# Performance work log

Measured on AMD Instinct MI355X. Metric: run time of the kernel, lower is better.

## Reference

```python
import jax, jax.numpy as jnp
import numpy as np
from functools import partial

V, H, B, T, L = 32000, 1024, 64, 64, 4
EOS = 2


def setup_inputs() -> dict:
    key = jax.random.key(0)
    ks = jax.random.split(key, 10)
    s = 1.0 / np.sqrt(H)
    return {
        "max_len": T,
        "tgt": jax.random.randint(ks[0], (B, T), 0, V),
        "h0": jax.random.normal(ks[1], (L, B, H), jnp.float32),
        "c0": jax.random.normal(ks[2], (L, B, H), jnp.float32),
        "embedding": jax.random.normal(ks[3], (V, H), jnp.float32) * s,
        "W_ih": jax.random.normal(ks[4], (L, 4 * H, H), jnp.float32) * s,
        "W_hh": jax.random.normal(ks[5], (L, 4 * H, H), jnp.float32) * s,
        "b_ih": jax.random.normal(ks[6], (L, 4 * H), jnp.float32) * s,
        "b_hh": jax.random.normal(ks[7], (L, 4 * H), jnp.float32) * s,
        "W_cls": jax.random.normal(ks[8], (V, H), jnp.float32) * s,
        "b_cls": jax.random.normal(ks[9], (V,), jnp.float32) * s,
    }


def _lstm_cell(x, h, c, Wi, Wh, bi, bh):
    # gates: [B, 4H] in torch order (i, f, g, o)
    g = x @ Wi.T + bi + h @ Wh.T + bh
    i, f, gg, o = jnp.split(g, 4, axis=-1)
    c2 = jax.nn.sigmoid(f) * c + jax.nn.sigmoid(i) * jnp.tanh(gg)
    h2 = jax.nn.sigmoid(o) * jnp.tanh(c2)
    return h2, c2


def reference(max_len, tgt, h0, c0, embedding, W_ih, W_hh, b_ih, b_hh, W_cls, b_cls):
    # step i>0 uses embedding of tgt[:, i-1].
    batch = tgt.shape[0]
    x0 = jnp.broadcast_to(embedding[EOS], (batch, embedding.shape[1]))
    tf_in = embedding[tgt[:, : max_len - 1]]              # [B, T-1, H]
    inputs = jnp.concatenate([x0[:, None, :], tf_in], axis=1)  # [B, T, H]
    inputs = jnp.swapaxes(inputs, 0, 1)                   # [T, B, H]

    def step(carry, x):
        h, c = carry  # each [L, B, H]
        hs, cs = [], []
        inp = x
        for l in range(L):  # 4 stacked LSTM cells, h of cell l feeds cell l+1
            hn, cn = _lstm_cell(inp, h[l], c[l], W_ih[l], W_hh[l], b_ih[l], b_hh[l])
            hs.append(hn)
            cs.append(cn)
            inp = hn
        h = jnp.stack(hs)
        c = jnp.stack(cs)
        logp = jax.nn.log_softmax(h[L - 1] @ W_cls.T + b_cls, axis=-1)  # [B, V]
        return (h, c), logp

    (h, c), out = jax.lax.scan(step, (h0, c0), inputs)
    return out, h, c  # out: [T, B, V]
```

## Files before the change

### kernel.cpp

```cpp
#include <hip/hip_runtime.h>

using u16 = unsigned short;
using u32 = unsigned int;

typedef __bf16 bf16x8 __attribute__((ext_vector_type(8)));
typedef float  f32x4  __attribute__((ext_vector_type(4)));
typedef u16    u16x8  __attribute__((ext_vector_type(8)));

static constexpr int kV = 32000, kH = 1024, kB = 64, kT = 64, kL = 4, kEOS = 2;

struct Flag { int v; int pad[15]; };

__device__ __forceinline__ u16 f2bf(float f) {
  u32 u = __float_as_uint(f);
  u = (u + 0x7fffu + ((u >> 16) & 1u)) >> 16;
  return (u16)u;
}
__device__ __forceinline__ float sigf(float x)   { return 1.0f / (1.0f + __expf(-x)); }
__device__ __forceinline__ float tanhf_(float x) { return 1.0f - 2.0f / (__expf(2.0f * x) + 1.0f); }

typedef const __attribute__((address_space(1))) u32* gas_ptr;
typedef __attribute__((address_space(3))) u32*       las_ptr;
__device__ __forceinline__ void async16(const u16* g, u16* l) {
  __builtin_amdgcn_global_load_lds((gas_ptr)g, (las_ptr)l, 16, 0, 0);
}

__device__ __forceinline__ void spin_ge(const int* p, int tgt) {
  while (__hip_atomic_load(p, __ATOMIC_RELAXED, __HIP_MEMORY_SCOPE_AGENT) < tgt)
    __builtin_amdgcn_s_sleep(2);
}

__device__ __forceinline__ size_t packed_off(int b, int k) {
  return (size_t)(((b >> 4) * 32 + (k >> 5)) * 512 + (((k >> 3) & 3) * 16 + (b & 15)) * 8 + (k & 7));
}


__global__ void pack_lstm(const float* __restrict__ Wih, const float* __restrict__ Whh,
                          u16* __restrict__ wpack) {
  const int cid  = blockIdx.x * 256 + threadIdx.x;
  const int lane = cid & 63;
  const int cf   = (cid >> 6) & 3;
  const int kk   = (cid >> 8) & 31;
  const int mt   = (cid >> 13) & 1;
  const int blk  = cid >> 14;
  const int lay = blk >> 6, cb = blk & 63;
  const int wr = cf * 1024 + cb * 16 + (lane & 15);
  const int kb = kk * 32 + (lane >> 4) * 8;
  const float* src = (mt ? Whh : Wih) + ((size_t)lay * 4096 + wr) * 1024 + kb;
  const float4* s4 = (const float4*)src;
  float4 v0 = s4[0], v1 = s4[1];
  u16x8 r;
  r[0]=f2bf(v0.x); r[1]=f2bf(v0.y); r[2]=f2bf(v0.z); r[3]=f2bf(v0.w);
  r[4]=f2bf(v1.x); r[5]=f2bf(v1.y); r[6]=f2bf(v1.z); r[7]=f2bf(v1.w);
  *(u16x8*)(wpack + (size_t)cid * 8) = r;
}

__global__ void pack_cls(const float* __restrict__ W, u16* __restrict__ o) {
  const int cid = blockIdx.x * 256 + threadIdx.x;
  const int bn  = cid >> 14;
  const int rem = cid & 16383;
  const int kk  = rem >> 9;
  const int p   = rem & 511;
  const int l4  = p >> 7;
  const int row = p & 127;
  const float* src = W + ((size_t)(bn * 128 + row)) * 1024 + kk * 32 + l4 * 8;
  const float4* s4 = (const float4*)src;
  float4 v0 = s4[0], v1 = s4[1];
  u16x8 r;
  r[0]=f2bf(v0.x); r[1]=f2bf(v0.y); r[2]=f2bf(v0.z); r[3]=f2bf(v0.w);
  r[4]=f2bf(v1.x); r[5]=f2bf(v1.y); r[6]=f2bf(v1.z); r[7]=f2bf(v1.w);
  *(u16x8*)(o + (size_t)cid * 8) = r;
}

__global__ void pack_x(const float* __restrict__ emb, const int* __restrict__ tgt,
                       u16* __restrict__ X) {
  const int cid = blockIdx.x * 256 + threadIdx.x;
  const int kc = cid & 127, b = (cid >> 7) & 63, t = cid >> 13;
  const int tok = (t == 0) ? kEOS : tgt[b * 64 + t - 1];
  const float4* s4 = (const float4*)(emb + (size_t)tok * 1024 + kc * 8);
  float4 v0 = s4[0], v1 = s4[1];
  u16x8 r;
  r[0]=f2bf(v0.x); r[1]=f2bf(v0.y); r[2]=f2bf(v0.z); r[3]=f2bf(v0.w);
  r[4]=f2bf(v1.x); r[5]=f2bf(v1.y); r[6]=f2bf(v1.z); r[7]=f2bf(v1.w);
  *(u16x8*)(X + (size_t)t * 65536 + packed_off(b, kc * 8)) = r;
}

__global__ void pack_init(const float* __restrict__ h0, const float* __restrict__ bih,
                          const float* __restrict__ bhh, u16* __restrict__ hball,
                          float* __restrict__ bsum) {
  const int cid = blockIdx.x * 256 + threadIdx.x;
  if (cid < 32768) {
    const int kc = cid & 127, row = cid >> 7;
    const int lay = row >> 6, b = row & 63;
    const float4* s4 = (const float4*)(h0 + (size_t)cid * 8);
    float4 v0 = s4[0], v1 = s4[1];
    u16x8 r;
    r[0]=f2bf(v0.x); r[1]=f2bf(v0.y); r[2]=f2bf(v0.z); r[3]=f2bf(v0.w);
    r[4]=f2bf(v1.x); r[5]=f2bf(v1.y); r[6]=f2bf(v1.z); r[7]=f2bf(v1.w);
    *(u16x8*)(hball + (size_t)lay * 65 * 65536 + packed_off(b, kc * 8)) = r;
  } else {
    const int i = cid - 32768;
    bsum[i] = bih[i] + bhh[i];
  }
}

__global__ void __launch_bounds__(1024, 4)
lstm_coop(const u16* __restrict__ wpack, const u16* __restrict__ xall,
          u16* __restrict__ hball, const float* __restrict__ bsum,
          const float* __restrict__ c0, float* __restrict__ outh, float* __restrict__ outc,
          Flag* flags) {
  __shared__ u16 stg[3][32][512];
  __shared__ float Gc[2][64][80];

  const int tid = threadIdx.x, lane = tid & 63, wave = tid >> 6;
  const int l15 = lane & 15, l4 = lane >> 4;
  const int cmat = wave >> 3, cwc = (wave >> 1) & 3, ckh = wave & 1;
  const int blk = blockIdx.x;
  const int lay = (blk >> 1) & 3;
  const int cb  = ((blk >> 3) << 1) | (blk & 1);
  const int u0 = cb << 4;
  const int ub = tid >> 4, uu = tid & 15;

  float creg = c0[((size_t)lay * 64 + ub) * 1024 + u0 + uu];
  float bsv[4];
  #pragma unroll
  for (int g = 0; g < 4; ++g) bsv[g] = bsum[lay * 4096 + g * 1024 + u0 + uu];

  const size_t wbase = (size_t)(lay * 64 + cb) * 131072;
  bf16x8 breg[16];
  #pragma unroll
  for (int j = 0; j < 16; ++j)
    breg[j] = *(const bf16x8*)(wpack + wbase
        + (size_t)(((cmat * 32 + 2 * j + ckh) * 4) + cwc) * 512 + lane * 8);

  const int j0 = wave * 2, j1 = wave * 2 + 1;
  const int m2a = j0 >> 4, mta = (j0 >> 2) & 3, ksla = j0 & 3;
  const int m2b = j1 >> 4, mtb = (j1 >> 2) & 3, kslb = j1 & 3;

  u16* hlay = hball + (size_t)lay * 65 * 65536;
  const u16* hprev = (lay == 0) ? xall : (hball + (size_t)(lay - 1) * 65 * 65536);

  #pragma unroll 1
  for (int t = 0; t < kT; ++t) {
    if (t > 0 && tid < 64)                 spin_ge(&flags[lay * 64 + tid].v, t);
    if (lay > 0 && tid >= 64 && tid < 128) spin_ge(&flags[(lay - 1) * 64 + (tid - 64)].v, t + 1);
    __syncthreads();

    const u16* xsrc = (lay == 0) ? (xall + (size_t)t * 65536)
                                 : (hprev + (size_t)(t + 1) * 65536);
    const u16* hsrc = hlay + (size_t)t * 65536;

    const u16* ga = (m2a ? hsrc : xsrc) + (size_t)((mta * 32 + ksla) * 512) + lane * 8;
    const u16* gb = (m2b ? hsrc : xsrc) + (size_t)((mtb * 32 + kslb) * 512) + lane * 8;

    auto STAGE = [&](int c) {
      async16(ga + (size_t)c * 2048, &stg[c % 3][m2a * 16 + mta * 4 + ksla][0]);
      async16(gb + (size_t)c * 2048, &stg[c % 3][m2b * 16 + mtb * 4 + kslb][0]);
    };

    f32x4 acc[4] = {};
    STAGE(0); STAGE(1);
    #pragma unroll
    for (int c = 0; c < 8; ++c) {
      if (c < 7) asm volatile("s_waitcnt vmcnt(2)" ::: "memory");
      else       asm volatile("s_waitcnt vmcnt(0)" ::: "memory");
      __builtin_amdgcn_s_barrier();
      asm volatile("" ::: "memory");
      if (c < 6) STAGE(c + 2);
      const u16* As = &stg[c % 3][cmat * 16][0];
      #pragma unroll
      for (int s = 0; s < 2; ++s) {
        const int ksl = 2 * s + ckh;
        bf16x8 a[4];
        #pragma unroll
        for (int m = 0; m < 4; ++m)
          a[m] = *(const bf16x8*)(As + (m * 4 + ksl) * 512 + lane * 8);
        #pragma unroll
        for (int m = 0; m < 4; ++m)
          acc[m] = __builtin_amdgcn_mfma_f32_16x16x32_bf16(a[m], breg[2 * c + s], acc[m], 0, 0, 0);
      }
    }

    if (ckh == 0) {
      #pragma unroll
      for (int m = 0; m < 4; ++m)
        #pragma unroll
        for (int r = 0; r < 4; ++r)
          Gc[cmat][m * 16 + l4 * 4 + r][cwc * 16 + l15] = acc[m][r];
    }
    __syncthreads();
    if (ckh == 1) {
      #pragma unroll
      for (int m = 0; m < 4; ++m)
        #pragma unroll
        for (int r = 0; r < 4; ++r)
          Gc[cmat][m * 16 + l4 * 4 + r][cwc * 16 + l15] += acc[m][r];
    }
    __syncthreads();

    float sg[4];
    #pragma unroll
    for (int g = 0; g < 4; ++g) {
      const int col = g * 16 + uu;
      sg[g] = Gc[0][ub][col] + Gc[1][ub][col] + bsv[g];
    }
    const float c2 = sigf(sg[1]) * creg + sigf(sg[0]) * tanhf_(sg[2]);
    const float h2 = sigf(sg[3]) * tanhf_(c2);
    creg = c2;
    const u16 hv = f2bf(h2);
    if (t == kT - 1) {
      outh[((size_t)lay * 64 + ub) * 1024 + u0 + uu] = h2;
      outc[((size_t)lay * 64 + ub) * 1024 + u0 + uu] = c2;
    }
    const u32 other = __shfl_xor((u32)hv, 1);
    if ((tid & 1) == 0) {
      const u32 hpair = (u32)hv | (other << 16);
      u32* hdst = (u32*)(hlay + (size_t)(t + 1) * 65536 + packed_off(ub, u0 + uu));
      __hip_atomic_store(hdst, hpair, __ATOMIC_RELAXED, __HIP_MEMORY_SCOPE_AGENT);
    }
    __syncthreads();
    if (tid == 0)
      __hip_atomic_store(&flags[lay * 64 + cb].v, t + 1, __ATOMIC_RELAXED, __HIP_MEMORY_SCOPE_AGENT);
  }
}

#define CLS_EPILOGUE()                                                                     \
  {                                                                                        \
    float* sRm = (float*)&sA[0][0];                                          \
    float* sRs = sRm + 256;                                                                \
    _Pragma("unroll")                                                                      \
    for (int mi = 0; mi < 4; ++mi) {                                                       \
      _Pragma("unroll")                                                                    \
      for (int r = 0; r < 4; ++r) {                                                        \
        float v[4];                                                                        \
        _Pragma("unroll")                                                                  \
        for (int ci = 0; ci < 4; ++ci) v[ci] = acc[mi][ci][r] + bc[ci];                     \
        float mx = fmaxf(fmaxf(v[0], v[1]), fmaxf(v[2], v[3]));                            \
        mx = fmaxf(mx, __shfl_xor(mx, 1)); mx = fmaxf(mx, __shfl_xor(mx, 2));              \
        mx = fmaxf(mx, __shfl_xor(mx, 4)); mx = fmaxf(mx, __shfl_xor(mx, 8));              \
        float ss = __expf(v[0]-mx) + __expf(v[1]-mx) + __expf(v[2]-mx) + __expf(v[3]-mx);  \
        ss += __shfl_xor(ss, 1); ss += __shfl_xor(ss, 2);                                  \
        ss += __shfl_xor(ss, 4); ss += __shfl_xor(ss, 8);                                  \
        const int lr = wm * 64 + mi * 16 + l4 * 4 + r;                                     \
        if (l15 == 0) { sRm[wc * 128 + lr] = mx; sRs[wc * 128 + lr] = ss; }                \
      }                                                                                    \
    }                                                                                      \
    __syncthreads();                                                                       \
    if (tid < 128) {                                                                       \
      const float m0 = sRm[tid], s0 = sRs[tid];                                            \
      const float m1 = sRm[128 + tid], s1 = sRs[128 + tid];                                \
      const float M = fmaxf(m0, m1);                                                       \
      const float S = s0 * __expf(m0 - M) + s1 * __expf(m1 - M);                           \
      pmax[(size_t)(bm * 128 + tid) * 256 + bn] = M;                                       \
      psum[(size_t)(bm * 128 + tid) * 256 + bn] = S;                                       \
    }                                                                                      \
  }

__global__ void __launch_bounds__(256)
cls_gemm(const u16* __restrict__ A, const u16* __restrict__ Bw,
         const float* __restrict__ bcls, float* __restrict__ out,
         float* __restrict__ pmax, float* __restrict__ psum) {
  __shared__ u16 sA[3][4096], sB[3][4096];
  const int tid = threadIdx.x, lane = tid & 63, wave = tid >> 6;
  const int wm = wave >> 1, wc = wave & 1;
  const int l15 = lane & 15, l4 = lane >> 4;
  const int bm = blockIdx.x, bn = blockIdx.y;
  const u16* Ab = A  + (size_t)bm * 131072;
  const u16* Bb = Bw + (size_t)bn * 131072;

  auto STAGE = [&](int kk) {
    u16* dA = sA[kk % 3]; u16* dB = sB[kk % 3];
    #pragma unroll
    for (int q = 0; q < 4; ++q) {
      const int u = wave * 4 + q;
      if (u < 8) {
        const u16* g = Ab + (size_t)(u >> 2) * 65536 + (size_t)(((u & 3) * 32 + kk) * 512) + lane * 8;
        async16(g, dA + u * 512);
      } else {
        const int v = u & 7;
        const u16* g = Bb + (size_t)kk * 4096 + v * 512 + lane * 8;
        async16(g, dB + v * 512);
      }
    }
  };

  f32x4 acc[4][4] = {};
  STAGE(0); STAGE(1);
  for (int kk = 0; kk < 32; ++kk) {
    if (kk < 31) asm volatile("s_waitcnt vmcnt(4)" ::: "memory");
    else         asm volatile("s_waitcnt vmcnt(0)" ::: "memory");
    __builtin_amdgcn_s_barrier();
    asm volatile("" ::: "memory");
    if (kk < 30) STAGE(kk + 2);
    const u16* aS = sA[kk % 3]; const u16* bS = sB[kk % 3];
    bf16x8 av[4], bv[4];
    #pragma unroll
    for (int mi = 0; mi < 4; ++mi) av[mi] = *(const bf16x8*)(aS + (wm * 4 + mi) * 512 + lane * 8);
    #pragma unroll
    for (int ci = 0; ci < 4; ++ci) bv[ci] = *(const bf16x8*)(bS + l4 * 1024 + (wc * 64 + ci * 16 + l15) * 8);
    #pragma unroll
    for (int mi = 0; mi < 4; ++mi)
      #pragma unroll
      for (int ci = 0; ci < 4; ++ci)
        acc[mi][ci] = __builtin_amdgcn_mfma_f32_16x16x32_bf16(av[mi], bv[ci], acc[mi][ci], 0, 0, 0);
  }
  float bc[4];
  #pragma unroll
  for (int ci = 0; ci < 4; ++ci) bc[ci] = bcls[bn * 128 + wc * 64 + ci * 16 + l15];
  #pragma unroll
  for (int ci = 0; ci < 4; ++ci) {
    const int col = bn * 128 + wc * 64 + ci * 16 + l15;
    #pragma unroll
    for (int mi = 0; mi < 4; ++mi)
      #pragma unroll
      for (int r = 0; r < 4; ++r) {
        const int row = bm * 128 + wm * 64 + mi * 16 + l4 * 4 + r;
        out[(size_t)row * 32000 + col] = acc[mi][ci][r] + bc[ci];
      }
  }
  __syncthreads();
  CLS_EPILOGUE()
}

__global__ void __launch_bounds__(256)
cls_gemm_f32(const u16* __restrict__ A, const float* __restrict__ Bw,
             const float* __restrict__ bcls, float* __restrict__ out,
             float* __restrict__ pmax, float* __restrict__ psum) {
  __shared__ u16 sA[3][4096], sB[3][4096];
  const int tid = threadIdx.x, lane = tid & 63, wave = tid >> 6;
  const int wm = wave >> 1, wc = wave & 1;
  const int l15 = lane & 15, l4 = lane >> 4;
  const int bm = blockIdx.x, bn = blockIdx.y;
  const u16*  Ab = A  + (size_t)bm * 131072;
  const float* Bb = Bw + (size_t)bn * 131072;

  auto LOADB = [&](int kk, u16x8* rb) {
    #pragma unroll
    for (int q = 0; q < 2; ++q) {
      const int p = tid + q * 256, row = p & 127, khi = p >> 7;
      const float4* s4 = (const float4*)(Bb + (size_t)row * 1024 + kk * 32 + khi * 8);
      float4 v0 = s4[0], v1 = s4[1];
      u16x8 r;
      r[0]=f2bf(v0.x); r[1]=f2bf(v0.y); r[2]=f2bf(v0.z); r[3]=f2bf(v0.w);
      r[4]=f2bf(v1.x); r[5]=f2bf(v1.y); r[6]=f2bf(v1.z); r[7]=f2bf(v1.w);
      rb[q] = r;
    }
  };
  auto WRITEB = [&](int kk, const u16x8* rb) {
    u16* dB = sB[kk % 3];
    #pragma unroll
    for (int q = 0; q < 2; ++q) {
      const int p = tid + q * 256, row = p & 127, khi = p >> 7;
      *(u16x8*)(dB + khi * 1024 + row * 8) = rb[q];
    }
  };
  auto STAGE_A = [&](int kk) {
    u16* dA = sA[kk % 3];
    #pragma unroll
    for (int q = 0; q < 2; ++q) {
      const int v = wave * 2 + q;
      const u16* g = Ab + (size_t)(v >> 2) * 65536 + (size_t)(((v & 3) * 32 + kk) * 512) + lane * 8;
      async16(g, dA + v * 512);
    }
  };

  f32x4 acc[4][4] = {};
  {
    u16x8 rb[2];
    LOADB(0, rb); STAGE_A(0); WRITEB(0, rb);
  }
  for (int kk = 0; kk < 32; ++kk) {
    if (kk < 31) {
      u16x8 rb[2];
      LOADB(kk + 1, rb);
      STAGE_A(kk + 1);
      WRITEB(kk + 1, rb);
    } else {
      asm volatile("s_waitcnt vmcnt(0)" ::: "memory");
    }
    __builtin_amdgcn_s_barrier();
    asm volatile("" ::: "memory");
    const u16* aS = sA[kk % 3]; const u16* bS = sB[kk % 3];
    bf16x8 av[4], bv[4];
    #pragma unroll
    for (int mi = 0; mi < 4; ++mi) av[mi] = *(const bf16x8*)(aS + (wm * 4 + mi) * 512 + lane * 8);
    #pragma unroll
    for (int ci = 0; ci < 4; ++ci) bv[ci] = *(const bf16x8*)(bS + l4 * 1024 + (wc * 64 + ci * 16 + l15) * 8);
    #pragma unroll
    for (int mi = 0; mi < 4; ++mi)
      #pragma unroll
      for (int ci = 0; ci < 4; ++ci)
        acc[mi][ci] = __builtin_amdgcn_mfma_f32_16x16x32_bf16(av[mi], bv[ci], acc[mi][ci], 0, 0, 0);
    asm volatile("" ::: "memory");
    __builtin_amdgcn_s_barrier();
  }
  float bc[4];
  #pragma unroll
  for (int ci = 0; ci < 4; ++ci) bc[ci] = bcls[bn * 128 + wc * 64 + ci * 16 + l15];
  #pragma unroll
  for (int ci = 0; ci < 4; ++ci) {
    const int col = bn * 128 + wc * 64 + ci * 16 + l15;
    #pragma unroll
    for (int mi = 0; mi < 4; ++mi)
      #pragma unroll
      for (int r = 0; r < 4; ++r) {
        const int row = bm * 128 + wm * 64 + mi * 16 + l4 * 4 + r;
        out[(size_t)row * 32000 + col] = acc[mi][ci][r] + bc[ci];
      }
  }
  __syncthreads();
  CLS_EPILOGUE()
}

__global__ void __launch_bounds__(256)
lsm_red(const float* __restrict__ pmax, const float* __restrict__ psum,
        float* __restrict__ logz) {
  __shared__ float rm[256], rs[256];
  const int r = blockIdx.x, b = threadIdx.x;
  float m = -3.0e38f, s = 0.0f;
  if (b < 250) { m = pmax[(size_t)r * 256 + b]; s = psum[(size_t)r * 256 + b]; }
  rm[b] = m; rs[b] = s; __syncthreads();
  for (int st = 128; st > 0; st >>= 1) {
    if (b < st) {
      const float m2 = rm[b + st], s2 = rs[b + st];
      const float M = fmaxf(rm[b], m2);
      rs[b] = rs[b] * __expf(rm[b] - M) + s2 * __expf(m2 - M);
      rm[b] = M;
    }
    __syncthreads();
  }
  if (b == 0) logz[r] = rm[0] + logf(rs[0]);
}

__global__ void __launch_bounds__(256)
sub_k(float* __restrict__ out, const float* __restrict__ logz) {
  const int r = blockIdx.x;
  const float z = logz[r];
  float4* p = (float4*)(out + (size_t)r * 32000);
  for (int v = threadIdx.x; v < 8000; v += 256) {
    float4 x = p[v];
    x.x -= z; x.y -= z; x.z -= z; x.w -= z;
    p[v] = x;
  }
}

extern "C" void kernel_launch(void* const* d_in, const int* in_sizes, int n_in,
                              void* d_out, int out_size, void* d_ws, size_t ws_size,
                              hipStream_t stream) {
  (void)in_sizes; (void)n_in; (void)out_size;
  const int*   tgt  = (const int*)d_in[1];
  const float* h0   = (const float*)d_in[2];
  const float* c0   = (const float*)d_in[3];
  const float* emb  = (const float*)d_in[4];
  const float* Wih  = (const float*)d_in[5];
  const float* Whh  = (const float*)d_in[6];
  const float* bih  = (const float*)d_in[7];
  const float* bhh  = (const float*)d_in[8];
  const float* Wcls = (const float*)d_in[9];
  const float* bcls = (const float*)d_in[10];

  float* out  = (float*)d_out;
  float* outh = out + (size_t)kT * kB * kV;
  float* outc = outh + (size_t)kL * kB * kH;

  const size_t SZ_WPACK = 67108864;
  const size_t SZ_WCLS  = 65536000;
  const size_t SZ_X     = 8388608;
  const size_t SZ_HBALL = 34078720;
  const size_t SZ_BSUM  = 65536;
  const size_t SZ_FLAGS = 16384;
  const size_t SZ_PM    = 4194304;
  const size_t FULL_REQ = SZ_WPACK + SZ_WCLS + SZ_X + SZ_HBALL + SZ_BSUM + SZ_FLAGS + 2 * SZ_PM + 16384;
  const bool full = (ws_size >= FULL_REQ);

  char* ws = (char*)d_ws;
  size_t off = 0;
  u16* wpack = (u16*)(ws + off); off += SZ_WPACK;
  u16* wclsb = nullptr;
  if (full) { wclsb = (u16*)(ws + off); off += SZ_WCLS; }
  u16*   X     = (u16*)(ws + off); off += SZ_X;
  u16*   hball = (u16*)(ws + off); off += SZ_HBALL;
  float* bsum  = (float*)(ws + off); off += SZ_BSUM;
  Flag*  flags = (Flag*)(ws + off);  off += SZ_FLAGS;
  float* pmax  = (float*)(ws + off); off += SZ_PM;
  float* psum  = (float*)(ws + off); off += SZ_PM;
  float* logz  = (float*)(ws + off); off += 16384;

  pack_lstm<<<16384, 256, 0, stream>>>(Wih, Whh, wpack);
  if (full) pack_cls<<<16000, 256, 0, stream>>>(Wcls, wclsb);
  pack_x   <<<2048,  256, 0, stream>>>(emb, tgt, X);
  pack_init<<<192,   256, 0, stream>>>(h0, bih, bhh, hball, bsum);
  hipMemsetAsync(flags, 0, SZ_FLAGS, stream);

  void* args[] = { (void*)&wpack, (void*)&X, (void*)&hball, (void*)&bsum,
                   (void*)&c0, (void*)&outh, (void*)&outc, (void*)&flags };
  hipLaunchCooperativeKernel((const void*)lstm_coop, dim3(256), dim3(1024), args, 0, stream);

  const u16* h3a = hball + (size_t)3 * 65 * 65536 + 65536;
  if (full) cls_gemm    <<<dim3(32, 250), 256, 0, stream>>>(h3a, wclsb, bcls, out, pmax, psum);
  else      cls_gemm_f32<<<dim3(32, 250), 256, 0, stream>>>(h3a, Wcls,  bcls, out, pmax, psum);
  lsm_red<<<4096, 256, 0, stream>>>(pmax, psum, logz);
  sub_k  <<<4096, 256, 0, stream>>>(out, logz);
}
```

Measured before the change: 1.263 ms.

## Enlarge classifier GEMM M-tile to 256 rows and fuse logsumexp reduce with subtract

The bf16 classifier GEMM now computes 256x128 output tiles per block instead of 128x128. Each wave holds 8x4 MFMA accumulators, which halves how often the W_cls tiles are reloaded and halves the grid along M. The log-softmax row reduction and the logZ subtraction are merged into one kernel, removing one launch and the logz round trip. The cost is more registers and LDS per block, which may lower occupancy.

```diff
diff --git a/kernel.cpp b/kernel.cpp
--- a/kernel.cpp
+++ b/kernel.cpp
@@ -224,9 +224,104 @@
   }
 }
 
-#define CLS_EPILOGUE()                                                                     \
+__global__ void __launch_bounds__(256, 2)
+cls_gemm(const u16* __restrict__ A, const u16* __restrict__ Bw,
+         const float* __restrict__ bcls, float* __restrict__ out,
+         float* __restrict__ pmax, float* __restrict__ psum) {
+  __shared__ u16 sA[3][8192], sB[3][4096];
+  const int tid = threadIdx.x, lane = tid & 63, wave = tid >> 6;
+  const int wm = wave >> 1, wc = wave & 1;
+  const int l15 = lane & 15, l4 = lane >> 4;
+  const int bm = blockIdx.x, bn = blockIdx.y;
+  const u16* Ab = A  + (size_t)bm * 262144;
+  const u16* Bb = Bw + (size_t)bn * 131072;
+
+  auto STAGE = [&](int kk) {
+    u16* dA = sA[kk % 3]; u16* dB = sB[kk % 3];
+    #pragma unroll
+    for (int q = 0; q < 6; ++q) {
+      const int u = wave * 6 + q;
+      if (u < 16) {
+        const u16* g = Ab + (size_t)(u >> 2) * 65536 + (size_t)(((u & 3) * 32 + kk) * 512) + lane * 8;
+        async16(g, dA + u * 512);
+      } else {
+        const int v = u - 16;
+        const u16* g = Bb + (size_t)kk * 4096 + v * 512 + lane * 8;
+        async16(g, dB + v * 512);
+      }
+    }
+  };
+
+  f32x4 acc[8][4] = {};
+  STAGE(0); STAGE(1);
+  for (int kk = 0; kk < 32; ++kk) {
+    if (kk < 31) asm volatile("s_waitcnt vmcnt(6)" ::: "memory");
+    else         asm volatile("s_waitcnt vmcnt(0)" ::: "memory");
+    __builtin_amdgcn_s_barrier();
+    asm volatile("" ::: "memory");
+    if (kk < 30) STAGE(kk + 2);
+    const u16* aS = sA[kk % 3]; const u16* bS = sB[kk % 3];
+    bf16x8 av[8], bv[4];
+    #pragma unroll
+    for (int mi = 0; mi < 8; ++mi) av[mi] = *(const bf16x8*)(aS + (size_t)(wm * 8 + mi) * 512 + lane * 8);
+    #pragma unroll
+    for (int ci = 0; ci < 4; ++ci) bv[ci] = *(const bf16x8*)(bS + l4 * 1024 + (wc * 64 + ci * 16 + l15) * 8);
+    #pragma unroll
+    for (int mi = 0; mi < 8; ++mi)
+      #pragma unroll
+      for (int ci = 0; ci < 4; ++ci)
+        acc[mi][ci] = __builtin_amdgcn_mfma_f32_16x16x32_bf16(av[mi], bv[ci], acc[mi][ci], 0, 0, 0);
+  }
+  float bc[4];
+  #pragma unroll
+  for (int ci = 0; ci < 4; ++ci) bc[ci] = bcls[bn * 128 + wc * 64 + ci * 16 + l15];
+  #pragma unroll
+  for (int ci = 0; ci < 4; ++ci) {
+    const int col = bn * 128 + wc * 64 + ci * 16 + l15;
+    #pragma unroll
+    for (int mi = 0; mi < 8; ++mi)
+      #pragma unroll
+      for (int r = 0; r < 4; ++r) {
+        const int row = bm * 256 + wm * 128 + mi * 16 + l4 * 4 + r;
+        out[(size_t)row * 32000 + col] = acc[mi][ci][r] + bc[ci];
+      }
+  }
+  __syncthreads();
+  {
+    float* sRm = (float*)&sA[0][0];
+    float* sRs = sRm + 512;
+    #pragma unroll
+    for (int mi = 0; mi < 8; ++mi) {
+      #pragma unroll
+      for (int r = 0; r < 4; ++r) {
+        float v[4];
+        #pragma unroll
+        for (int ci = 0; ci < 4; ++ci) v[ci] = acc[mi][ci][r] + bc[ci];
+        float mx = fmaxf(fmaxf(v[0], v[1]), fmaxf(v[2], v[3]));
+        mx = fmaxf(mx, __shfl_xor(mx, 1)); mx = fmaxf(mx, __shfl_xor(mx, 2));
+        mx = fmaxf(mx, __shfl_xor(mx, 4)); mx = fmaxf(mx, __shfl_xor(mx, 8));
+        float ss = __expf(v[0]-mx) + __expf(v[1]-mx) + __expf(v[2]-mx) + __expf(v[3]-mx);
+        ss += __shfl_xor(ss, 1); ss += __shfl_xor(ss, 2);
+        ss += __shfl_xor(ss, 4); ss += __shfl_xor(ss, 8);
+        const int lr = wm * 128 + mi * 16 + l4 * 4 + r;
+        if (l15 == 0) { sRm[wc * 256 + lr] = mx; sRs[wc * 256 + lr] = ss; }
+      }
+    }
+    __syncthreads();
+    {
+      const float m0 = sRm[tid], s0 = sRs[tid];
+      const float m1 = sRm[256 + tid], s1 = sRs[256 + tid];
+      const float M = fmaxf(m0, m1);
+      const float S = s0 * __expf(m0 - M) + s1 * __expf(m1 - M);
+      pmax[(size_t)(bm * 256 + tid) * 256 + bn] = M;
+      psum[(size_t)(bm * 256 + tid) * 256 + bn] = S;
+    }
+  }
+}
+
+#define CLS_EPILOGUE_128()                                                                 \
   {                                                                                        \
-    float* sRm = (float*)&sA[0][0];                                          \
+    float* sRm = (float*)&sA[0][0];                                                        \
     float* sRs = sRm + 256;                                                                \
     _Pragma("unroll")                                                                      \
     for (int mi = 0; mi < 4; ++mi) {                                                       \
@@ -257,72 +352,6 @@
   }
 
 __global__ void __launch_bounds__(256)
-cls_gemm(const u16* __restrict__ A, const u16* __restrict__ Bw,
-         const float* __restrict__ bcls, float* __restrict__ out,
-         float* __restrict__ pmax, float* __restrict__ psum) {
-  __shared__ u16 sA[3][4096], sB[3][4096];
-  const int tid = threadIdx.x, lane = tid & 63, wave = tid >> 6;
-  const int wm = wave >> 1, wc = wave & 1;
-  const int l15 = lane & 15, l4 = lane >> 4;
-  const int bm = blockIdx.x, bn = blockIdx.y;
-  const u16* Ab = A  + (size_t)bm * 131072;
-  const u16* Bb = Bw + (size_t)bn * 131072;
-
-  auto STAGE = [&](int kk) {
-    u16* dA = sA[kk % 3]; u16* dB = sB[kk % 3];
-    #pragma unroll
-    for (int q = 0; q < 4; ++q) {
-      const int u = wave * 4 + q;
-      if (u < 8) {
-        const u16* g = Ab + (size_t)(u >> 2) * 65536 + (size_t)(((u & 3) * 32 + kk) * 512) + lane * 8;
-        async16(g, dA + u * 512);
-      } else {
-        const int v = u & 7;
-        const u16* g = Bb + (size_t)kk * 4096 + v * 512 + lane * 8;
-        async16(g, dB + v * 512);
-      }
-    }
-  };
-
-  f32x4 acc[4][4] = {};
-  STAGE(0); STAGE(1);
-  for (int kk = 0; kk < 32; ++kk) {
-    if (kk < 31) asm volatile("s_waitcnt vmcnt(4)" ::: "memory");
-    else         asm volatile("s_waitcnt vmcnt(0)" ::: "memory");
-    __builtin_amdgcn_s_barrier();
-    asm volatile("" ::: "memory");
-    if (kk < 30) STAGE(kk + 2);
-    const u16* aS = sA[kk % 3]; const u16* bS = sB[kk % 3];
-    bf16x8 av[4], bv[4];
-    #pragma unroll
-    for (int mi = 0; mi < 4; ++mi) av[mi] = *(const bf16x8*)(aS + (wm * 4 + mi) * 512 + lane * 8);
-    #pragma unroll
-    for (int ci = 0; ci < 4; ++ci) bv[ci] = *(const bf16x8*)(bS + l4 * 1024 + (wc * 64 + ci * 16 + l15) * 8);
-    #pragma unroll
-    for (int mi = 0; mi < 4; ++mi)
-      #pragma unroll
-      for (int ci = 0; ci < 4; ++ci)
-        acc[mi][ci] = __builtin_amdgcn_mfma_f32_16x16x32_bf16(av[mi], bv[ci], acc[mi][ci], 0, 0, 0);
-  }
-  float bc[4];
-  #pragma unroll
-  for (int ci = 0; ci < 4; ++ci) bc[ci] = bcls[bn * 128 + wc * 64 + ci * 16 + l15];
-  #pragma unroll
-  for (int ci = 0; ci < 4; ++ci) {
-    const int col = bn * 128 + wc * 64 + ci * 16 + l15;
-    #pragma unroll
-    for (int mi = 0; mi < 4; ++mi)
-      #pragma unroll
-      for (int r = 0; r < 4; ++r) {
-        const int row = bm * 128 + wm * 64 + mi * 16 + l4 * 4 + r;
-        out[(size_t)row * 32000 + col] = acc[mi][ci][r] + bc[ci];
-      }
-  }
-  __syncthreads();
-  CLS_EPILOGUE()
-}
-
-__global__ void __launch_bounds__(256)
 cls_gemm_f32(const u16* __restrict__ A, const float* __restrict__ Bw,
              const float* __restrict__ bcls, float* __restrict__ out,
              float* __restrict__ pmax, float* __restrict__ psum) {
@@ -409,12 +438,12 @@
       }
   }
   __syncthreads();
-  CLS_EPILOGUE()
+  CLS_EPILOGUE_128()
 }
 
 __global__ void __launch_bounds__(256)
-lsm_red(const float* __restrict__ pmax, const float* __restrict__ psum,
-        float* __restrict__ logz) {
+lsm_sub(const float* __restrict__ pmax, const float* __restrict__ psum,
+        float* __restrict__ out) {
   __shared__ float rm[256], rs[256];
   const int r = blockIdx.x, b = threadIdx.x;
   float m = -3.0e38f, s = 0.0f;
@@ -429,15 +458,9 @@
     }
     __syncthreads();
   }
-  if (b == 0) logz[r] = rm[0] + logf(rs[0]);
-}
-
-__global__ void __launch_bounds__(256)
-sub_k(float* __restrict__ out, const float* __restrict__ logz) {
-  const int r = blockIdx.x;
-  const float z = logz[r];
+  const float z = rm[0] + logf(rs[0]);
   float4* p = (float4*)(out + (size_t)r * 32000);
-  for (int v = threadIdx.x; v < 8000; v += 256) {
+  for (int v = b; v < 8000; v += 256) {
     float4 x = p[v];
     x.x -= z; x.y -= z; x.z -= z; x.w -= z;
     p[v] = x;
@@ -484,7 +507,6 @@
   Flag*  flags = (Flag*)(ws + off);  off += SZ_FLAGS;
   float* pmax  = (float*)(ws + off); off += SZ_PM;
   float* psum  = (float*)(ws + off); off += SZ_PM;
-  float* logz  = (float*)(ws + off); off += 16384;
 
   pack_lstm<<<16384, 256, 0, stream>>>(Wih, Whh, wpack);
   if (full) pack_cls<<<16000, 256, 0, stream>>>(Wcls, wclsb);
@@ -497,8 +519,7 @@
   hipLaunchCooperativeKernel((const void*)lstm_coop, dim3(256), dim3(1024), args, 0, stream);
 
   const u16* h3a = hball + (size_t)3 * 65 * 65536 + 65536;
-  if (full) cls_gemm    <<<dim3(32, 250), 256, 0, stream>>>(h3a, wclsb, bcls, out, pmax, psum);
+  if (full) cls_gemm    <<<dim3(16, 250), 256, 0, stream>>>(h3a, wclsb, bcls, out, pmax, psum);
   else      cls_gemm_f32<<<dim3(32, 250), 256, 0, stream>>>(h3a, Wcls,  bcls, out, pmax, psum);
-  lsm_red<<<4096, 256, 0, stream>>>(pmax, psum, logz);
-  sub_k  <<<4096, 256, 0, stream>>>(out, logz);
-}
+  lsm_sub<<<4096, 256, 0, stream>>>(pmax, psum, out);
+}
```

New measurement: 1.303 ms. 1.03x slower.
